# Kernel tuning notes

Hardware: AMD Instinct MI355X
Metric: run time of the kernel (lower is better)

The kernel has to match this reference:

```python
import jax, jax.numpy as jnp
import numpy as np

N = 2_000_000  # number of 3x3 SPD matrices (DTI-scale volume)


def _make_spd(key, n):
    # M M^T + 0.5 I is symmetric positive definite with generically distinct eigenvalues
    m = jax.random.normal(key, (n, 3, 3), dtype=jnp.float32)
    return m @ jnp.swapaxes(m, -1, -2) + 0.5 * jnp.eye(3, dtype=jnp.float32)


def setup_inputs() -> dict:
    key = jax.random.key(0)
    k1, k2 = jax.random.split(key)
    return {"D1": _make_spd(k1, N), "D2": _make_spd(k2, N)}


def _logm_spd(D):
    # Batched symmetric matrix log via eigendecomposition: V diag(log w) V^T
    w, v = jnp.linalg.eigh(D)                    # w: [N,3], v: [N,3,3]
    return (v * jnp.log(w)[..., None, :]) @ jnp.swapaxes(v, -1, -2)


def reference(D1, D2):
    # Log-Euclidean SPD distance: ||logm(D1) - logm(D2)||_F, then mean of squares
    diff = _logm_spd(D1) - _logm_spd(D2)         # [N,3,3]
    sq_dist = jnp.sum(diff * diff, axis=(-1, -2))  # [N]
    return jnp.mean(sq_dist)
```

## Files before the change

kernel.cpp:

```cpp
#include <hip/hip_runtime.h>
#include <hip/hip_bf16.h>

#define BLOCK 256
#define TILE 256
#define TILE_FLOATS (TILE * 9)
#define CHUNKS 18

__device__ __forceinline__ float frcp(float x) { return __builtin_amdgcn_rcpf(x); }
__device__ __forceinline__ float fsqrt(float x) { return __builtin_amdgcn_sqrtf(x); }

__device__ __forceinline__ float facos(float x) {
    float ax = fabsf(x);
    float sq = fsqrt(fmaxf(1.0f - ax, 0.0f));
    float poly = fmaf(fmaf(fmaf(-0.0187293f, ax, 0.0742610f), ax, -0.2121144f),
                      ax, 1.5707288f);
    float ac = sq * poly;
    return (x < 0.0f) ? (3.14159274f - ac) : ac;
}

__device__ __forceinline__ void logm3(const float m[6], float L[6]) {
    float a00 = m[0], a01 = m[1], a02 = m[2];
    float a11 = m[3], a12 = m[4], a22 = m[5];

    float q  = (a00 + a11 + a22) * (1.0f / 3.0f);
    float b00 = a00 - q, b11 = a11 - q, b22 = a22 - q;
    float p2 = b00*b00 + b11*b11 + b22*b22
             + 2.0f * (a01*a01 + a02*a02 + a12*a12);
    float p  = fsqrt(p2 * (1.0f / 6.0f));
    p = fmaxf(p, 1e-12f);
    float ip = frcp(p);
    float detB = b00*(b11*b22 - a12*a12)
               - a01*(a01*b22 - a12*a02)
               + a02*(a01*a12 - b11*a02);
    float ip3 = ip * ip * ip;
    float r = fminf(fmaxf(0.5f * detB * ip3, -1.0f), 1.0f);
    float phi = facos(r) * (1.0f / 3.0f);
    float sph = __sinf(phi), cph = __cosf(phi);
    float whi = q + 2.0f * p * cph;
    float wlo = q - p * (cph + 1.7320508f * sph);
    float wmid = 3.0f * q - whi - wlo;
    float w0 = fmaxf(wlo,  1e-8f);
    float w1 = fmaxf(wmid, 1e-8f);
    float w2 = fmaxf(whi,  1e-8f);

    float l0 = __logf(w0), l1 = __logf(w1), l2 = __logf(w2);
    float d01 = w1 - w0, d12 = w2 - w1, span = w2 - w0;
    float thr = 1e-3f * w1;
    float dd01 = (d01 > thr) ? (l1 - l0) * frcp(d01) : 2.0f * frcp(w0 + w1);
    float dd12 = (d12 > thr) ? (l2 - l1) * frcp(d12) : 2.0f * frcp(w1 + w2);
    float dd012 = (span > thr) ? (dd12 - dd01) * frcp(span)
                               : -0.5f * frcp(w1 * w1);
    float k2 = dd012;
    float k1 = dd01 - dd012 * (w0 + w1);
    float k0 = l0 - dd01 * w0 + dd012 * (w0 * w1);

    float s00 = a00*a00 + a01*a01 + a02*a02;
    float s01 = a00*a01 + a01*a11 + a02*a12;
    float s02 = a00*a02 + a01*a12 + a02*a22;
    float s11 = a01*a01 + a11*a11 + a12*a12;
    float s12 = a01*a02 + a11*a12 + a12*a22;
    float s22 = a02*a02 + a12*a12 + a22*a22;

    L[0] = k0 + k1*a00 + k2*s00;
    L[1] =      k1*a01 + k2*s01;
    L[2] =      k1*a02 + k2*s02;
    L[3] = k0 + k1*a11 + k2*s11;
    L[4] =      k1*a12 + k2*s12;
    L[5] = k0 + k1*a22 + k2*s22;
}

__device__ __forceinline__ void load6(const float* __restrict__ a, float m[6]) {
    m[0] = a[0]; m[1] = a[1]; m[2] = a[2];
    m[3] = a[4]; m[4] = a[5]; m[5] = a[8];
}

__device__ __forceinline__ float fnorm2_diff(const float L1[6], const float L2[6]) {
    float d0 = L1[0]-L2[0], d1 = L1[1]-L2[1], d2 = L1[2]-L2[2];
    float d3 = L1[3]-L2[3], d4 = L1[4]-L2[4], d5 = L1[5]-L2[5];
    return d0*d0 + d3*d3 + d5*d5 + 2.0f * (d1*d1 + d2*d2 + d4*d4);
}

__device__ __forceinline__ void issue_tile(float* buf,
                                           const float* __restrict__ D1,
                                           const float* __restrict__ D2,
                                           long t, int wave, int lane) {
    const float* s1 = D1 + t * TILE_FLOATS;
    const float* s2 = D2 + t * TILE_FLOATS;
    #pragma unroll
    for (int k = 0; k < 5; ++k) {
        int c = wave + k * 4;
        if (c < CHUNKS) {
            const float* g = (c < 9 ? s1 + c * 256 : s2 + (c - 9) * 256) + lane * 4;
            float* l = buf + c * 256;
            __builtin_amdgcn_global_load_lds(
                (const __attribute__((address_space(1))) unsigned int*)g,
                (__attribute__((address_space(3))) unsigned int*)l,
                16, 0, 0);
        }
    }
}

__global__ void __launch_bounds__(BLOCK)
le_partial(const float* __restrict__ D1, const float* __restrict__ D2,
           float* __restrict__ partial, int n, int ntiles) {
    __shared__ __align__(16) float lds[2 * 2 * TILE_FLOATS];
    const int tid  = threadIdx.x;
    const int wave = tid >> 6, lane = tid & 63;
    const int tstep = gridDim.x;
    float acc = 0.0f;

    long t = blockIdx.x;

    if (t < ntiles) issue_tile(lds, D1, D2, t, wave, lane);
    __syncthreads();

    int cur = 0;
    while (t < ntiles) {
        long tn = t + tstep;
        if (tn < ntiles)
            issue_tile(lds + (cur ^ 1) * (2 * TILE_FLOATS), D1, D2, tn, wave, lane);

        const float* b = lds + cur * (2 * TILE_FLOATS);
        float m1[6], m2[6], L1[6], L2[6];
        load6(b + tid * 9, m1);
        load6(b + TILE_FLOATS + tid * 9, m2);
        logm3(m1, L1);
        logm3(m2, L2);
        acc += fnorm2_diff(L1, L2);

        __syncthreads();
        cur ^= 1;
        t = tn;
    }

    {
        long ti = (long)ntiles * TILE + (long)blockIdx.x * BLOCK + tid;
        if (ti < n) {
            float m1[6], m2[6], L1[6], L2[6];
            load6(D1 + ti * 9, m1);
            load6(D2 + ti * 9, m2);
            logm3(m1, L1);
            logm3(m2, L2);
            acc += fnorm2_diff(L1, L2);
        }
    }

    #pragma unroll
    for (int off = 32; off > 0; off >>= 1)
        acc += __shfl_down(acc, off, 64);
    __shared__ float wsum[BLOCK / 64];
    if (lane == 0) wsum[wave] = acc;
    __syncthreads();
    if (tid == 0) {
        float s = 0.0f;
        #pragma unroll
        for (int j = 0; j < BLOCK / 64; ++j) s += wsum[j];
        partial[blockIdx.x] = s;
    }
}

__global__ void __launch_bounds__(BLOCK)
le_final(const float* __restrict__ partial, int nparts,
         float* __restrict__ out, double invN) {
    double s = 0.0;
    for (int i = threadIdx.x; i < nparts; i += BLOCK)
        s += (double)partial[i];
    #pragma unroll
    for (int off = 32; off > 0; off >>= 1)
        s += __shfl_down(s, off, 64);
    __shared__ double ws[BLOCK / 64];
    if ((threadIdx.x & 63) == 0) ws[threadIdx.x >> 6] = s;
    __syncthreads();
    if (threadIdx.x == 0) {
        double tt = 0.0;
        #pragma unroll
        for (int i = 0; i < BLOCK / 64; ++i) tt += ws[i];
        out[0] = (float)(tt * invN);
    }
}

extern "C" void kernel_launch(void* const* d_in, const int* in_sizes, int n_in,
                              void* d_out, int out_size, void* d_ws, size_t ws_size,
                              hipStream_t stream) {
    const float* D1 = (const float*)d_in[0];
    const float* D2 = (const float*)d_in[1];
    float* out = (float*)d_out;
    float* partial = (float*)d_ws;

    int n = in_sizes[0] / 9;
    int ntiles = n / TILE;

    int grid = 1024;
    if (ntiles > 0 && grid > ntiles) grid = ntiles;
    int maxblocks = (int)(ws_size / sizeof(float));
    if (maxblocks > 0 && grid > maxblocks) grid = maxblocks;
    if (grid < 1) grid = 1;

    le_partial<<<grid, BLOCK, 0, stream>>>(D1, D2, partial, n, ntiles);
    le_final<<<1, BLOCK, 0, stream>>>(partial, grid, out, 1.0 / (double)n);
}
```

Measured before the change: 33.24 us.

## Use per-wave double-buffered LDS tiles with vmcnt waits instead of block barriers

Each wave now streams its own 64-pair tiles into a private double buffer via global_load_lds, waiting only on its own outstanding loads with s_waitcnt vmcnt rather than a block-wide __syncthreads each iteration. This removes barrier stalls between waves in the main loop. Separately, the divided-difference computation for the log interpolation drops its branches: the gaps are clamped and a single reciprocal of their product replaces three. The clamp changes numerics for near-degenerate eigenvalues, and the hand-written vmcnt counts depend on the exact number of issued loads.

```diff
diff --git a/kernel.cpp b/kernel.cpp
--- a/kernel.cpp
+++ b/kernel.cpp
@@ -2,9 +2,10 @@
 #include <hip/hip_bf16.h>
 
 #define BLOCK 256
-#define TILE 256
-#define TILE_FLOATS (TILE * 9)
-#define CHUNKS 18
+#define NWAVES 4
+#define WPAIRS 64
+#define WTILE_FLOATS (WPAIRS * 9)
+#define WBUF_FLOATS (2 * WTILE_FLOATS)
 
 __device__ __forceinline__ float frcp(float x) { return __builtin_amdgcn_rcpf(x); }
 __device__ __forceinline__ float fsqrt(float x) { return __builtin_amdgcn_sqrtf(x); }
@@ -44,12 +45,14 @@
     float w2 = fmaxf(whi,  1e-8f);
 
     float l0 = __logf(w0), l1 = __logf(w1), l2 = __logf(w2);
-    float d01 = w1 - w0, d12 = w2 - w1, span = w2 - w0;
-    float thr = 1e-3f * w1;
-    float dd01 = (d01 > thr) ? (l1 - l0) * frcp(d01) : 2.0f * frcp(w0 + w1);
-    float dd12 = (d12 > thr) ? (l2 - l1) * frcp(d12) : 2.0f * frcp(w1 + w2);
-    float dd012 = (span > thr) ? (dd12 - dd01) * frcp(span)
-                               : -0.5f * frcp(w1 * w1);
+    float e = 1e-4f * w2;
+    float d01 = fmaxf(w1 - w0, e);
+    float d12 = fmaxf(w2 - w1, e);
+    float d02 = fmaxf(w2 - w0, e);
+    float rP = frcp(d01 * d12 * d02);
+    float dd01 = (l1 - l0) * (d12 * d02) * rP;
+    float dd12 = (l2 - l1) * (d01 * d02) * rP;
+    float dd012 = (dd12 - dd01) * (d01 * d12) * rP;
     float k2 = dd012;
     float k1 = dd01 - dd012 * (w0 + w1);
     float k0 = l0 - dd01 * w0 + dd012 * (w0 * w1);
@@ -80,62 +83,74 @@
     return d0*d0 + d3*d3 + d5*d5 + 2.0f * (d1*d1 + d2*d2 + d4*d4);
 }
 
-__device__ __forceinline__ void issue_tile(float* buf,
-                                           const float* __restrict__ D1,
-                                           const float* __restrict__ D2,
-                                           long t, int wave, int lane) {
-    const float* s1 = D1 + t * TILE_FLOATS;
-    const float* s2 = D2 + t * TILE_FLOATS;
-    #pragma unroll
-    for (int k = 0; k < 5; ++k) {
-        int c = wave + k * 4;
-        if (c < CHUNKS) {
-            const float* g = (c < 9 ? s1 + c * 256 : s2 + (c - 9) * 256) + lane * 4;
-            float* l = buf + c * 256;
-            __builtin_amdgcn_global_load_lds(
-                (const __attribute__((address_space(1))) unsigned int*)g,
-                (__attribute__((address_space(3))) unsigned int*)l,
-                16, 0, 0);
-        }
-    }
+__device__ __forceinline__ void gld_lds16(const float* g, float* l) {
+    __builtin_amdgcn_global_load_lds(
+        (const __attribute__((address_space(1))) unsigned int*)g,
+        (__attribute__((address_space(3))) unsigned int*)l, 16, 0, 0);
+}
+__device__ __forceinline__ void gld_lds4(const float* g, float* l) {
+    __builtin_amdgcn_global_load_lds(
+        (const __attribute__((address_space(1))) unsigned int*)g,
+        (__attribute__((address_space(3))) unsigned int*)l, 4, 0, 0);
+}
+
+__device__ __forceinline__ void issue_wtile(float* buf,
+                                            const float* __restrict__ D1,
+                                            const float* __restrict__ D2,
+                                            long t, int lane) {
+    const float* s1 = D1 + t * WTILE_FLOATS;
+    const float* s2 = D2 + t * WTILE_FLOATS;
+    gld_lds16(s1 +       lane * 4, buf);
+    gld_lds16(s1 + 256 + lane * 4, buf + 256);
+    gld_lds4 (s1 + 512 + lane,     buf + 512);
+    gld_lds16(s2 +       lane * 4, buf + 576);
+    gld_lds16(s2 + 256 + lane * 4, buf + 832);
+    gld_lds4 (s2 + 512 + lane,     buf + 1088);
 }
 
 __global__ void __launch_bounds__(BLOCK)
 le_partial(const float* __restrict__ D1, const float* __restrict__ D2,
-           float* __restrict__ partial, int n, int ntiles) {
-    __shared__ __align__(16) float lds[2 * 2 * TILE_FLOATS];
+           float* __restrict__ partial, int n) {
+    __shared__ __align__(16) float lds[NWAVES * 2 * WBUF_FLOATS];
     const int tid  = threadIdx.x;
     const int wave = tid >> 6, lane = tid & 63;
-    const int tstep = gridDim.x;
+    float* wlds = lds + wave * (2 * WBUF_FLOATS);
+
+    const long ntw = n / WPAIRS;
+    const long W   = (long)gridDim.x * NWAVES;
+    long t = (long)blockIdx.x * NWAVES + wave;
     float acc = 0.0f;
 
-    long t = blockIdx.x;
-
-    if (t < ntiles) issue_tile(lds, D1, D2, t, wave, lane);
-    __syncthreads();
-
-    int cur = 0;
-    while (t < ntiles) {
-        long tn = t + tstep;
-        if (tn < ntiles)
-            issue_tile(lds + (cur ^ 1) * (2 * TILE_FLOATS), D1, D2, tn, wave, lane);
-
-        const float* b = lds + cur * (2 * TILE_FLOATS);
-        float m1[6], m2[6], L1[6], L2[6];
-        load6(b + tid * 9, m1);
-        load6(b + TILE_FLOATS + tid * 9, m2);
-        logm3(m1, L1);
-        logm3(m2, L2);
-        acc += fnorm2_diff(L1, L2);
-
-        __syncthreads();
-        cur ^= 1;
-        t = tn;
+    if (t < ntw) {
+        issue_wtile(wlds, D1, D2, t, lane);
+        int cur = 0;
+        while (true) {
+            long tn = t + W;
+            bool hn = (tn < ntw);
+            if (hn) issue_wtile(wlds + (cur ^ 1) * WBUF_FLOATS, D1, D2, tn, lane);
+
+            if (hn) asm volatile("s_waitcnt vmcnt(6)" ::: "memory");
+            else    asm volatile("s_waitcnt vmcnt(0)" ::: "memory");
+            __builtin_amdgcn_sched_barrier(0);
+
+            const float* b = wlds + cur * WBUF_FLOATS;
+            float m1[6], m2[6], L1[6], L2[6];
+            load6(b + lane * 9, m1);
+            load6(b + WTILE_FLOATS + lane * 9, m2);
+            logm3(m1, L1);
+            logm3(m2, L2);
+            acc += fnorm2_diff(L1, L2);
+
+            if (!hn) break;
+            cur ^= 1;
+            t = tn;
+        }
     }
 
     {
-        long ti = (long)ntiles * TILE + (long)blockIdx.x * BLOCK + tid;
-        if (ti < n) {
+        long base = ntw * WPAIRS;
+        if (blockIdx.x == 0 && (long)tid < n - base) {
+            long ti = base + tid;
             float m1[6], m2[6], L1[6], L2[6];
             load6(D1 + ti * 9, m1);
             load6(D2 + ti * 9, m2);
@@ -148,13 +163,13 @@
     #pragma unroll
     for (int off = 32; off > 0; off >>= 1)
         acc += __shfl_down(acc, off, 64);
-    __shared__ float wsum[BLOCK / 64];
+    __shared__ float wsum[NWAVES];
     if (lane == 0) wsum[wave] = acc;
     __syncthreads();
     if (tid == 0) {
         float s = 0.0f;
         #pragma unroll
-        for (int j = 0; j < BLOCK / 64; ++j) s += wsum[j];
+        for (int j = 0; j < NWAVES; ++j) s += wsum[j];
         partial[blockIdx.x] = s;
     }
 }
@@ -188,14 +203,15 @@
     float* partial = (float*)d_ws;
 
     int n = in_sizes[0] / 9;
-    int ntiles = n / TILE;
+    long ntw = n / WPAIRS;
 
     int grid = 1024;
-    if (ntiles > 0 && grid > ntiles) grid = ntiles;
+    long maxg = (ntw + NWAVES - 1) / NWAVES;
+    if (maxg > 0 && grid > maxg) grid = (int)maxg;
     int maxblocks = (int)(ws_size / sizeof(float));
     if (maxblocks > 0 && grid > maxblocks) grid = maxblocks;
     if (grid < 1) grid = 1;
 
-    le_partial<<<grid, BLOCK, 0, stream>>>(D1, D2, partial, n, ntiles);
+    le_partial<<<grid, BLOCK, 0, stream>>>(D1, D2, partial, n);
     le_final<<<1, BLOCK, 0, stream>>>(partial, grid, out, 1.0 / (double)n);
 }
```

After: 33.54 us. Within noise of the previous version (+0.9%).
